# Performance work log

Measured on AMD Instinct MI355X. Metric: run time of the kernel, lower is better.

The kernel has to match this reference:

```python
import jax, jax.numpy as jnp
import numpy as np

N_ENT = 100000
N_REL = 500
N_EDGES = 800000
IN_DIM = 128
OUT_DIM = 128


def setup_inputs() -> dict:
    key = jax.random.key(0)
    ks = jax.random.split(key, 7)
    heads = jax.random.randint(ks[0], (N_EDGES,), 0, N_ENT)
    tails = jax.random.randint(ks[1], (N_EDGES,), 0, N_ENT)
    rels = jax.random.randint(ks[2], (N_EDGES,), 0, N_REL)
    triplets = jnp.stack([heads, tails, rels], axis=1)  # [E, 3] (head, tail, rel)
    ent_embed = jax.random.normal(ks[3], (N_ENT, IN_DIM), dtype=jnp.float32)
    rel_embed = jax.random.normal(ks[4], (N_REL, IN_DIM), dtype=jnp.float32)
    # xavier_normal with gain=1.414 for both linear weights; zero biases (torch default bias init is uniform, but scale is tiny)
    Wa = jax.random.normal(ks[5], (OUT_DIM, 3 * IN_DIM), dtype=jnp.float32) * (1.414 * np.sqrt(2.0 / (3 * IN_DIM + OUT_DIM)))
    Wa2 = jax.random.normal(ks[6], (1, OUT_DIM), dtype=jnp.float32) * (1.414 * np.sqrt(2.0 / (OUT_DIM + 1)))
    ba = jnp.zeros((OUT_DIM,), dtype=jnp.float32)
    ba2 = jnp.zeros((1,), dtype=jnp.float32)
    return {"triplets": triplets, "ent_embed": ent_embed, "rel_embed": rel_embed,
            "Wa": Wa, "ba": ba, "Wa2": Wa2, "ba2": ba2}


def reference(triplets, ent_embed, rel_embed, Wa, ba, Wa2, ba2):
    heads = triplets[:, 0]
    tails = triplets[:, 1]
    rels = triplets[:, 2]
    # gather per-edge features: [E, 3*in_dim]
    h = jnp.concatenate([ent_embed[heads], rel_embed[rels], ent_embed[tails]], axis=1)
    c = h @ Wa.T + ba                      # [E, out_dim]
    b = jax.nn.leaky_relu(c @ Wa2.T + ba2)  # [E, 1], slope 0.01 (torch default)
    e_b = jnp.exp(b)                       # [E, 1]
    # torch builds sparse COO (head, rel) tensors, detaches, and sums over dim=1:
    # that is exactly a segment-sum over head node. detach -> stop_gradient.
    ebs = jax.ops.segment_sum(jax.lax.stop_gradient(e_b), heads, num_segments=N_ENT)       # [N, 1]
    hs = jax.ops.segment_sum(jax.lax.stop_gradient(e_b * c), heads, num_segments=N_ENT)    # [N, out_dim]
    ebs = jnp.where(ebs == 0.0, jnp.float32(1e-12), ebs)
    out = hs / ebs
    return jax.nn.elu(out)  # concat=True branch
```

## Files before the change

kernel.cpp:

```cpp
#include <hip/hip_runtime.h>

#define N_ENT   100000
#define N_REL   500
#define N_EDGES 800000
#define DIM     128
#define WA_LD   384

#define MT       256
#define ENT_BLKS ((N_ENT + MT - 1) / MT)
#define REL_BLKS 63
#define CAP      64

#define SCW 264

typedef __attribute__((ext_vector_type(8))) short  s8v;
typedef __attribute__((ext_vector_type(4))) float  f4v;

__device__ __forceinline__ unsigned short f2bf(float x) {
    unsigned u = __float_as_uint(x);
    return (unsigned short)((u + 0x7FFFu + ((u >> 16) & 1u)) >> 16);
}
__device__ __forceinline__ float bf2f(unsigned short h) {
    return __uint_as_float(((unsigned)h) << 16);
}

__global__ __launch_bounds__(512) void k_prep(const float* __restrict__ Wa,
                                              short* __restrict__ Bg) {
    int t = threadIdx.x;
#pragma unroll
    for (int tt = 0; tt < 2; ++tt) {
#pragma unroll
        for (int it = 0; it < 4; ++it) {
            int g = t + 512 * it;
            int j = g >> 4;
            int k8 = g & 15;
            const float* src = Wa + (size_t)j * WA_LD + tt * 256 + k8 * 8;
            float4 v0 = *(const float4*)src;
            float4 v1 = *(const float4*)(src + 4);
            float x[8] = {v0.x, v0.y, v0.z, v0.w, v1.x, v1.y, v1.z, v1.w};
            s8v hv;
#pragma unroll
            for (int e = 0; e < 8; ++e) hv[e] = (short)f2bf(x[e]);
            int col = tt * 128 + j;
            int kc = k8 >> 2;
            int lanep = (k8 & 3) * 16 + (col & 15);
            int nt = col >> 4;
            *(s8v*)&Bg[((size_t)((kc * 16 + nt) * 64 + lanep)) * 8] = hv;
        }
    }
}

__global__ __launch_bounds__(512) void k_fused(const float* __restrict__ ent,
                                               const short* __restrict__ Bg,
                                               const float* __restrict__ Wa2,
                                               unsigned short* __restrict__ PHb,
                                               unsigned short* __restrict__ PTb,
                                               float* __restrict__ qh,
                                               float* __restrict__ qt,
                                               const float* __restrict__ rel,
                                               const float* __restrict__ Wa,
                                               const float* __restrict__ ba,
                                               float* __restrict__ PR,
                                               float* __restrict__ qr) {
    __shared__ __align__(16) unsigned short SCR[8 * 16 * SCW];
    __shared__ float relLds[8][128];
    s8v* BsV = (s8v*)SCR;
    int t = threadIdx.x;
    int wv = t >> 6;
    int lane = t & 63;

    if (blockIdx.x >= ENT_BLKS) {
        int rb = blockIdx.x - ENT_BLKS;
        int r = rb * 8 + wv;
        if (r < N_REL) {
            relLds[wv][lane]      = rel[r * DIM + lane];
            relLds[wv][64 + lane] = rel[r * DIM + 64 + lane];
            int j0 = 2 * lane, j1 = j0 + 1;
            const float* w0 = Wa + (size_t)j0 * WA_LD + 128;
            const float* w1 = Wa + (size_t)j1 * WA_LD + 128;
            float a0 = ba[j0], a1 = ba[j1];
#pragma unroll 8
            for (int k4 = 0; k4 < 32; ++k4) {
                float4 rv = *(const float4*)&relLds[wv][4 * k4];
                float4 x0 = *(const float4*)&w0[4 * k4];
                float4 x1 = *(const float4*)&w1[4 * k4];
                a0 += rv.x * x0.x + rv.y * x0.y + rv.z * x0.z + rv.w * x0.w;
                a1 += rv.x * x1.x + rv.y * x1.y + rv.z * x1.z + rv.w * x1.w;
            }
            *(float2*)&PR[(size_t)r * DIM + j0] = make_float2(a0, a1);
            float p = a0 * Wa2[j0] + a1 * Wa2[j1];
#pragma unroll
            for (int m = 1; m <= 32; m <<= 1) p += __shfl_xor(p, m);
            if (lane == 0) qr[r] = p;
        }
        return;
    }

#pragma unroll
    for (int it = 0; it < 8; ++it) {
        int idx = t + 512 * it;
        BsV[idx] = *(const s8v*)&Bg[(size_t)idx * 8];
    }

    int l15 = lane & 15, lg = lane >> 4;
    int m0 = blockIdx.x * MT + wv * 32;

    f4v acc[2][16];
#pragma unroll
    for (int s = 0; s < 2; ++s)
#pragma unroll
        for (int nt = 0; nt < 16; ++nt)
            acc[s][nt] = (f4v){0.f, 0.f, 0.f, 0.f};

    __syncthreads();

#pragma unroll
    for (int kc = 0; kc < 4; ++kc) {
        s8v Ah[2];
#pragma unroll
        for (int s = 0; s < 2; ++s) {
            int row = m0 + s * 16 + l15;
            if (row < N_ENT) {
                const float* ap = ent + (size_t)row * DIM + kc * 32 + lg * 8;
                float4 v0 = *(const float4*)ap;
                float4 v1 = *(const float4*)(ap + 4);
                float x[8] = {v0.x, v0.y, v0.z, v0.w, v1.x, v1.y, v1.z, v1.w};
#pragma unroll
                for (int e = 0; e < 8; ++e) Ah[s][e] = (short)f2bf(x[e]);
            } else {
                Ah[s] = (s8v){0, 0, 0, 0, 0, 0, 0, 0};
            }
        }
#pragma unroll
        for (int nt = 0; nt < 16; ++nt) {
            s8v bg = BsV[(kc * 16 + nt) * 64 + lane];
            acc[0][nt] = __builtin_amdgcn_mfma_f32_16x16x32_bf16(Ah[0], bg, acc[0][nt], 0, 0, 0);
            acc[1][nt] = __builtin_amdgcn_mfma_f32_16x16x32_bf16(Ah[1], bg, acc[1][nt], 0, 0, 0);
        }
    }

    float wa2v[8];
#pragma unroll
    for (int c8 = 0; c8 < 8; ++c8) wa2v[c8] = Wa2[c8 * 16 + l15];

#pragma unroll
    for (int s = 0; s < 2; ++s) {
        int rowb = m0 + s * 16 + lg * 4;
        float qhp[4] = {0.f, 0.f, 0.f, 0.f};
        float qtp[4] = {0.f, 0.f, 0.f, 0.f};
#pragma unroll
        for (int nt = 0; nt < 16; ++nt) {
#pragma unroll
            for (int g = 0; g < 4; ++g) {
                float v = acc[s][nt][g];
                if (nt < 8) qhp[g] += v * wa2v[nt];
                else        qtp[g] += v * wa2v[nt & 7];
            }
        }
#pragma unroll
        for (int g = 0; g < 4; ++g) {
            float a = qhp[g], b = qtp[g];
#pragma unroll
            for (int m = 1; m <= 8; m <<= 1) {
                a += __shfl_xor(a, m);
                b += __shfl_xor(b, m);
            }
            int row = rowb + g;
            if (l15 == 0 && row < N_ENT) { qh[row] = a; qt[row] = b; }
        }
    }

    __syncthreads();

    unsigned short* scr = &SCR[wv * 16 * SCW];
#pragma unroll
    for (int s = 0; s < 2; ++s) {
#pragma unroll
        for (int nt = 0; nt < 16; ++nt)
#pragma unroll
            for (int g = 0; g < 4; ++g)
                scr[(lg * 4 + g) * SCW + nt * 16 + l15] = f2bf(acc[s][nt][g]);
#pragma unroll
        for (int p = 0; p < 8; ++p) {
            int row16 = p * 2 + (lane >> 5);
            int col8  = lane & 31;
            s8v val = *(s8v*)&scr[row16 * SCW + col8 * 8];
            int row = m0 + s * 16 + row16;
            if (row < N_ENT) {
                unsigned short* dst = (col8 < 16 ? PHb : PTb)
                                    + (size_t)row * DIM + (col8 & 15) * 8;
                *(s8v*)dst = val;
            }
        }
    }
}

__global__ __launch_bounds__(256) void k_scatter(const int* __restrict__ trip,
                                                 const float* __restrict__ qh,
                                                 const float* __restrict__ qt,
                                                 const float* __restrict__ qr,
                                                 const float* __restrict__ ba2,
                                                 int* __restrict__ cnt,
                                                 float2* __restrict__ pkw) {
    __shared__ int tl3[768];
    int t = threadIdx.x;
    int e0blk = blockIdx.x * 256;
    int base3 = e0blk * 3;
#pragma unroll
    for (int i = t; i < 768; i += 256)
        tl3[i] = (base3 + i < N_EDGES * 3) ? trip[base3 + i] : 0;
    __syncthreads();
    int e = e0blk + t;
    if (e >= N_EDGES) return;
    int h  = tl3[t * 3 + 0];
    int tt = tl3[t * 3 + 1];
    int r  = tl3[t * 3 + 2];
    float b = qh[h] + qt[tt] + qr[r] + ba2[0];
    float lr = b > 0.f ? b : 0.01f * b;
    float w = expf(lr);
    int pos = atomicAdd(&cnt[h], 1);
    if (pos < CAP) {
        float2 v;
        v.x = __uint_as_float(((unsigned)r << 17) | (unsigned)tt);
        v.y = w;
        pkw[(size_t)h * CAP + pos] = v;
    }
}

__global__ __launch_bounds__(256) void k_gather(const int* __restrict__ cnt,
                                                const float2* __restrict__ pkw,
                                                const unsigned short* __restrict__ PHb,
                                                const float* __restrict__ PR,
                                                const unsigned short* __restrict__ PTb,
                                                float* __restrict__ out) {
    int idx = blockIdx.x * 256 + threadIdx.x;
    int i = idx >> 5, lane = idx & 31;
    if (i >= N_ENT) return;
    int lane4 = lane * 4;
    int e0 = i * CAP;
    int n = cnt[i]; if (n > CAP) n = CAP;
    int e1 = e0 + n;
    float4 acc = make_float4(0.f, 0.f, 0.f, 0.f);
    float sw = 0.f;
    int e = e0;
    for (; e + 3 < e1; e += 4) {
        float2 pw0 = pkw[e],     pw1 = pkw[e + 1];
        float2 pw2 = pkw[e + 2], pw3 = pkw[e + 3];
        unsigned p0 = __float_as_uint(pw0.x), p1 = __float_as_uint(pw1.x);
        unsigned p2 = __float_as_uint(pw2.x), p3 = __float_as_uint(pw3.x);
        ushort4 b0 = *(const ushort4*)&PTb[(size_t)(p0 & 0x1FFFFu) * DIM + lane4];
        ushort4 b1 = *(const ushort4*)&PTb[(size_t)(p1 & 0x1FFFFu) * DIM + lane4];
        ushort4 b2 = *(const ushort4*)&PTb[(size_t)(p2 & 0x1FFFFu) * DIM + lane4];
        ushort4 b3 = *(const ushort4*)&PTb[(size_t)(p3 & 0x1FFFFu) * DIM + lane4];
        float4 r0 = *(const float4*)&PR[(size_t)(p0 >> 17) * DIM + lane4];
        float4 r1 = *(const float4*)&PR[(size_t)(p1 >> 17) * DIM + lane4];
        float4 r2 = *(const float4*)&PR[(size_t)(p2 >> 17) * DIM + lane4];
        float4 r3 = *(const float4*)&PR[(size_t)(p3 >> 17) * DIM + lane4];
        float w0 = pw0.y, w1 = pw1.y, w2 = pw2.y, w3 = pw3.y;
        acc.x += w0 * (r0.x + bf2f(b0.x)) + w1 * (r1.x + bf2f(b1.x))
               + w2 * (r2.x + bf2f(b2.x)) + w3 * (r3.x + bf2f(b3.x));
        acc.y += w0 * (r0.y + bf2f(b0.y)) + w1 * (r1.y + bf2f(b1.y))
               + w2 * (r2.y + bf2f(b2.y)) + w3 * (r3.y + bf2f(b3.y));
        acc.z += w0 * (r0.z + bf2f(b0.z)) + w1 * (r1.z + bf2f(b1.z))
               + w2 * (r2.z + bf2f(b2.z)) + w3 * (r3.z + bf2f(b3.z));
        acc.w += w0 * (r0.w + bf2f(b0.w)) + w1 * (r1.w + bf2f(b1.w))
               + w2 * (r2.w + bf2f(b2.w)) + w3 * (r3.w + bf2f(b3.w));
        sw += (w0 + w1) + (w2 + w3);
    }
    for (; e < e1; ++e) {
        float2 pw = pkw[e];
        unsigned p = __float_as_uint(pw.x);
        float w = pw.y;
        ushort4 b = *(const ushort4*)&PTb[(size_t)(p & 0x1FFFFu) * DIM + lane4];
        float4 pr = *(const float4*)&PR[(size_t)(p >> 17) * DIM + lane4];
        acc.x += w * (pr.x + bf2f(b.x));
        acc.y += w * (pr.y + bf2f(b.y));
        acc.z += w * (pr.z + bf2f(b.z));
        acc.w += w * (pr.w + bf2f(b.w));
        sw += w;
    }
    ushort4 hb = *(const ushort4*)&PHb[(size_t)i * DIM + lane4];
    acc.x += sw * bf2f(hb.x);
    acc.y += sw * bf2f(hb.y);
    acc.z += sw * bf2f(hb.z);
    acc.w += sw * bf2f(hb.w);
    float den = (sw == 0.f) ? 1e-12f : sw;
    float inv = 1.f / den;
    float vx = acc.x * inv, vy = acc.y * inv, vz = acc.z * inv, vw = acc.w * inv;
    vx = vx > 0.f ? vx : expm1f(vx);
    vy = vy > 0.f ? vy : expm1f(vy);
    vz = vz > 0.f ? vz : expm1f(vz);
    vw = vw > 0.f ? vw : expm1f(vw);
    *(float4*)&out[(size_t)i * DIM + lane4] = make_float4(vx, vy, vz, vw);
}

extern "C" void kernel_launch(void* const* d_in, const int* in_sizes, int n_in,
                              void* d_out, int out_size, void* d_ws, size_t ws_size,
                              hipStream_t stream) {
    const int*   trip = (const int*)d_in[0];
    const float* ent  = (const float*)d_in[1];
    const float* rel  = (const float*)d_in[2];
    const float* Wa   = (const float*)d_in[3];
    const float* ba   = (const float*)d_in[4];
    const float* Wa2  = (const float*)d_in[5];
    const float* ba2  = (const float*)d_in[6];
    float* out = (float*)d_out;

    float* ws = (float*)d_ws;
    size_t o = 0;
    unsigned short* PHb = (unsigned short*)(ws + o); o += (size_t)N_ENT * DIM / 2;
    unsigned short* PTb = (unsigned short*)(ws + o); o += (size_t)N_ENT * DIM / 2;
    float* PR = ws + o;        o += (size_t)N_REL * DIM;
    float* qh = ws + o;        o += N_ENT;
    float* qt = ws + o;        o += N_ENT;
    float* qr = ws + o;        o += N_REL + 4;
    short* Bg = (short*)(ws + o);     o += 32768 / 2 + 8;
    int*   cnt = (int*)(ws + o);      o += N_ENT;
    float2* pkw = (float2*)(ws + o);  o += (size_t)N_ENT * CAP * 2;

    hipMemsetAsync(cnt, 0, (size_t)N_ENT * sizeof(int), stream);

    k_prep<<<1, 512, 0, stream>>>(Wa, Bg);
    k_fused<<<ENT_BLKS + REL_BLKS, 512, 0, stream>>>(ent, Bg, Wa2, PHb, PTb, qh, qt,
                                                     rel, Wa, ba, PR, qr);
    k_scatter<<<(N_EDGES + 255) / 256, 256, 0, stream>>>(trip, qh, qt, qr, ba2, cnt, pkw);
    k_gather<<<(N_ENT * 32) / 256, 256, 0, stream>>>(cnt, pkw, PHb, PR, PTb, out);
}
```

Baseline: 141.3 us.

## Move edge weight computation into gather and shrink scatter payload to packed indices

The scatter kernel now stores only the packed (rel, tail) index per edge and no longer depends on the projection outputs, so it is launched before the fused projection kernel. The edge weight (leaky-relu then exp of qh+qt+qr+bias) is recomputed inside the gather kernel, with qr staged in shared memory. The weight-prep kernel is spread over 16 blocks instead of one. This halves the per-edge bucket traffic and removes a dependency, at the cost of an extra random qt load and an exp per edge per lane in the gather loop (repeated across all 32 lanes).

New measurement: 152.9 us. 1.08x slower.

```diff
diff --git a/kernel.cpp b/kernel.cpp
--- a/kernel.cpp
+++ b/kernel.cpp
@@ -24,30 +24,25 @@
     return __uint_as_float(((unsigned)h) << 16);
 }
 
-__global__ __launch_bounds__(512) void k_prep(const float* __restrict__ Wa,
+__global__ __launch_bounds__(256) void k_prep(const float* __restrict__ Wa,
                                               short* __restrict__ Bg) {
-    int t = threadIdx.x;
-#pragma unroll
-    for (int tt = 0; tt < 2; ++tt) {
-#pragma unroll
-        for (int it = 0; it < 4; ++it) {
-            int g = t + 512 * it;
-            int j = g >> 4;
-            int k8 = g & 15;
-            const float* src = Wa + (size_t)j * WA_LD + tt * 256 + k8 * 8;
-            float4 v0 = *(const float4*)src;
-            float4 v1 = *(const float4*)(src + 4);
-            float x[8] = {v0.x, v0.y, v0.z, v0.w, v1.x, v1.y, v1.z, v1.w};
-            s8v hv;
-#pragma unroll
-            for (int e = 0; e < 8; ++e) hv[e] = (short)f2bf(x[e]);
-            int col = tt * 128 + j;
-            int kc = k8 >> 2;
-            int lanep = (k8 & 3) * 16 + (col & 15);
-            int nt = col >> 4;
-            *(s8v*)&Bg[((size_t)((kc * 16 + nt) * 64 + lanep)) * 8] = hv;
-        }
-    }
+    int idx = blockIdx.x * 256 + threadIdx.x;
+    int tt = idx >> 11;
+    int g = idx & 2047;
+    int j = g >> 4;
+    int k8 = g & 15;
+    const float* src = Wa + (size_t)j * WA_LD + tt * 256 + k8 * 8;
+    float4 v0 = *(const float4*)src;
+    float4 v1 = *(const float4*)(src + 4);
+    float x[8] = {v0.x, v0.y, v0.z, v0.w, v1.x, v1.y, v1.z, v1.w};
+    s8v hv;
+#pragma unroll
+    for (int e = 0; e < 8; ++e) hv[e] = (short)f2bf(x[e]);
+    int col = tt * 128 + j;
+    int kc = k8 >> 2;
+    int lanep = (k8 & 3) * 16 + (col & 15);
+    int nt = col >> 4;
+    *(s8v*)&Bg[((size_t)((kc * 16 + nt) * 64 + lanep)) * 8] = hv;
 }
 
 __global__ __launch_bounds__(512) void k_fused(const float* __restrict__ ent,
@@ -196,12 +191,8 @@
 }
 
 __global__ __launch_bounds__(256) void k_scatter(const int* __restrict__ trip,
-                                                 const float* __restrict__ qh,
-                                                 const float* __restrict__ qt,
-                                                 const float* __restrict__ qr,
-                                                 const float* __restrict__ ba2,
                                                  int* __restrict__ cnt,
-                                                 float2* __restrict__ pkw) {
+                                                 unsigned* __restrict__ pk) {
     __shared__ int tl3[768];
     int t = threadIdx.x;
     int e0blk = blockIdx.x * 256;
@@ -215,48 +206,59 @@
     int h  = tl3[t * 3 + 0];
     int tt = tl3[t * 3 + 1];
     int r  = tl3[t * 3 + 2];
-    float b = qh[h] + qt[tt] + qr[r] + ba2[0];
-    float lr = b > 0.f ? b : 0.01f * b;
-    float w = expf(lr);
     int pos = atomicAdd(&cnt[h], 1);
-    if (pos < CAP) {
-        float2 v;
-        v.x = __uint_as_float(((unsigned)r << 17) | (unsigned)tt);
-        v.y = w;
-        pkw[(size_t)h * CAP + pos] = v;
-    }
+    if (pos < CAP)
+        pk[(size_t)h * CAP + pos] = ((unsigned)r << 17) | (unsigned)tt;
 }
 
 __global__ __launch_bounds__(256) void k_gather(const int* __restrict__ cnt,
-                                                const float2* __restrict__ pkw,
+                                                const unsigned* __restrict__ pk,
                                                 const unsigned short* __restrict__ PHb,
                                                 const float* __restrict__ PR,
                                                 const unsigned short* __restrict__ PTb,
+                                                const float* __restrict__ qh,
+                                                const float* __restrict__ qt,
+                                                const float* __restrict__ qr,
+                                                const float* __restrict__ ba2,
                                                 float* __restrict__ out) {
-    int idx = blockIdx.x * 256 + threadIdx.x;
+    __shared__ float qrs[N_REL];
+    int t = threadIdx.x;
+    for (int i = t; i < N_REL; i += 256) qrs[i] = qr[i];
+    __syncthreads();
+    int idx = blockIdx.x * 256 + t;
     int i = idx >> 5, lane = idx & 31;
     if (i >= N_ENT) return;
     int lane4 = lane * 4;
     int e0 = i * CAP;
     int n = cnt[i]; if (n > CAP) n = CAP;
     int e1 = e0 + n;
+    float qb = qh[i] + ba2[0];
     float4 acc = make_float4(0.f, 0.f, 0.f, 0.f);
     float sw = 0.f;
     int e = e0;
     for (; e + 3 < e1; e += 4) {
-        float2 pw0 = pkw[e],     pw1 = pkw[e + 1];
-        float2 pw2 = pkw[e + 2], pw3 = pkw[e + 3];
-        unsigned p0 = __float_as_uint(pw0.x), p1 = __float_as_uint(pw1.x);
-        unsigned p2 = __float_as_uint(pw2.x), p3 = __float_as_uint(pw3.x);
-        ushort4 b0 = *(const ushort4*)&PTb[(size_t)(p0 & 0x1FFFFu) * DIM + lane4];
-        ushort4 b1 = *(const ushort4*)&PTb[(size_t)(p1 & 0x1FFFFu) * DIM + lane4];
-        ushort4 b2 = *(const ushort4*)&PTb[(size_t)(p2 & 0x1FFFFu) * DIM + lane4];
-        ushort4 b3 = *(const ushort4*)&PTb[(size_t)(p3 & 0x1FFFFu) * DIM + lane4];
-        float4 r0 = *(const float4*)&PR[(size_t)(p0 >> 17) * DIM + lane4];
-        float4 r1 = *(const float4*)&PR[(size_t)(p1 >> 17) * DIM + lane4];
-        float4 r2 = *(const float4*)&PR[(size_t)(p2 >> 17) * DIM + lane4];
-        float4 r3 = *(const float4*)&PR[(size_t)(p3 >> 17) * DIM + lane4];
-        float w0 = pw0.y, w1 = pw1.y, w2 = pw2.y, w3 = pw3.y;
+        unsigned p0 = pk[e],     p1 = pk[e + 1];
+        unsigned p2 = pk[e + 2], p3 = pk[e + 3];
+        int t0 = (int)(p0 & 0x1FFFFu), r0_ = (int)(p0 >> 17);
+        int t1 = (int)(p1 & 0x1FFFFu), r1_ = (int)(p1 >> 17);
+        int t2 = (int)(p2 & 0x1FFFFu), r2_ = (int)(p2 >> 17);
+        int t3 = (int)(p3 & 0x1FFFFu), r3_ = (int)(p3 >> 17);
+        ushort4 b0 = *(const ushort4*)&PTb[(size_t)t0 * DIM + lane4];
+        ushort4 b1 = *(const ushort4*)&PTb[(size_t)t1 * DIM + lane4];
+        ushort4 b2 = *(const ushort4*)&PTb[(size_t)t2 * DIM + lane4];
+        ushort4 b3 = *(const ushort4*)&PTb[(size_t)t3 * DIM + lane4];
+        float4 r0 = *(const float4*)&PR[(size_t)r0_ * DIM + lane4];
+        float4 r1 = *(const float4*)&PR[(size_t)r1_ * DIM + lane4];
+        float4 r2 = *(const float4*)&PR[(size_t)r2_ * DIM + lane4];
+        float4 r3 = *(const float4*)&PR[(size_t)r3_ * DIM + lane4];
+        float bb0 = qb + qt[t0] + qrs[r0_];
+        float bb1 = qb + qt[t1] + qrs[r1_];
+        float bb2 = qb + qt[t2] + qrs[r2_];
+        float bb3 = qb + qt[t3] + qrs[r3_];
+        float w0 = expf(bb0 > 0.f ? bb0 : 0.01f * bb0);
+        float w1 = expf(bb1 > 0.f ? bb1 : 0.01f * bb1);
+        float w2 = expf(bb2 > 0.f ? bb2 : 0.01f * bb2);
+        float w3 = expf(bb3 > 0.f ? bb3 : 0.01f * bb3);
         acc.x += w0 * (r0.x + bf2f(b0.x)) + w1 * (r1.x + bf2f(b1.x))
                + w2 * (r2.x + bf2f(b2.x)) + w3 * (r3.x + bf2f(b3.x));
         acc.y += w0 * (r0.y + bf2f(b0.y)) + w1 * (r1.y + bf2f(b1.y))
@@ -268,11 +270,12 @@
         sw += (w0 + w1) + (w2 + w3);
     }
     for (; e < e1; ++e) {
-        float2 pw = pkw[e];
-        unsigned p = __float_as_uint(pw.x);
-        float w = pw.y;
-        ushort4 b = *(const ushort4*)&PTb[(size_t)(p & 0x1FFFFu) * DIM + lane4];
-        float4 pr = *(const float4*)&PR[(size_t)(p >> 17) * DIM + lane4];
+        unsigned p = pk[e];
+        int tt = (int)(p & 0x1FFFFu), rr = (int)(p >> 17);
+        ushort4 b = *(const ushort4*)&PTb[(size_t)tt * DIM + lane4];
+        float4 pr = *(const float4*)&PR[(size_t)rr * DIM + lane4];
+        float bb = qb + qt[tt] + qrs[rr];
+        float w = expf(bb > 0.f ? bb : 0.01f * bb);
         acc.x += w * (pr.x + bf2f(b.x));
         acc.y += w * (pr.y + bf2f(b.y));
         acc.z += w * (pr.z + bf2f(b.z));
@@ -316,13 +319,14 @@
     float* qr = ws + o;        o += N_REL + 4;
     short* Bg = (short*)(ws + o);     o += 32768 / 2 + 8;
     int*   cnt = (int*)(ws + o);      o += N_ENT;
-    float2* pkw = (float2*)(ws + o);  o += (size_t)N_ENT * CAP * 2;
+    unsigned* pk = (unsigned*)(ws + o); o += (size_t)N_ENT * CAP;
 
     hipMemsetAsync(cnt, 0, (size_t)N_ENT * sizeof(int), stream);
 
-    k_prep<<<1, 512, 0, stream>>>(Wa, Bg);
+    k_prep<<<16, 256, 0, stream>>>(Wa, Bg);
+    k_scatter<<<(N_EDGES + 255) / 256, 256, 0, stream>>>(trip, cnt, pk);
     k_fused<<<ENT_BLKS + REL_BLKS, 512, 0, stream>>>(ent, Bg, Wa2, PHb, PTb, qh, qt,
                                                      rel, Wa, ba, PR, qr);
-    k_scatter<<<(N_EDGES + 255) / 256, 256, 0, stream>>>(trip, qh, qt, qr, ba2, cnt, pkw);
-    k_gather<<<(N_ENT * 32) / 256, 256, 0, stream>>>(cnt, pkw, PHb, PR, PTb, out);
-}
+    k_gather<<<(N_ENT * 32) / 256, 256, 0, stream>>>(cnt, pk, PHb, PR, PTb,
+                                                     qh, qt, qr, ba2, out);
+}
```
